# Kernel optimization log

Hardware: AMD Instinct MI355X
Metric: run time of the kernel (lower is better)

Reference implementation:

```python
import jax, jax.numpy as jnp
import numpy as np
from jax import lax

NEG = -1e9
B, H, C, TX, TY = 4, 256, 80, 256, 1024  # batch, hidden, mel bins, text len, mel len


def setup_inputs() -> dict:
    key = jax.random.key(0)
    k = jax.random.split(key, 6)
    en = jax.random.normal(k[0], (B, H, TX), jnp.float32)
    mu = jax.random.normal(k[1], (B, C, TX), jnp.float32)
    log_sigma = 0.1 * jax.random.normal(k[2], (B, C, TX), jnp.float32)
    y = jax.random.normal(k[3], (B, C, TY), jnp.float32)
    x_lengths = jax.random.randint(k[4], (B,), TX // 2, TX + 1, jnp.int32)
    y_lengths = jax.random.randint(k[5], (B,), TY // 2, TY + 1, jnp.int32)
    return {"en": en, "mu": mu, "log_sigma": log_sigma, "y": y,
            "x_lengths": x_lengths, "y_lengths": y_lengths}


def sequence_mask(lengths, max_len):
    return jnp.arange(max_len)[None, :] < lengths[:, None]


def compute_log_probs(mu, log_sigma, y):
    # y: [B,C,Ty] -> [B,1,Ty,C]; mu/log_sigma: [B,C,Tx] -> [B,Tx,1,C]
    yb = jnp.transpose(y, (0, 2, 1))[:, None]
    mub = jnp.transpose(mu, (0, 2, 1))[:, :, None]
    lsb = jnp.transpose(log_sigma, (0, 2, 1))[:, :, None]
    # mse / sigma^2 = (y-mu)^2 * exp(-2*log_sigma); mean over channel dim
    expo = -0.5 * jnp.mean((yb - mub) ** 2 * jnp.exp(-2.0 * lsb), axis=-1)  # [B,Tx,Ty]
    return expo - 0.5 * jnp.mean(lsb, axis=-1)  # broadcast [B,Tx,1] -> [B,Tx,Ty]


def maximum_path(logp, mask, x_lengths, y_lengths):
    """Monotonic alignment search (Glow-TTS Viterbi DP), vectorized over batch."""
    b, tx, ty = logp.shape
    lp = jnp.where(mask > 0, logp, NEG)
    cols = jnp.moveaxis(lp, 2, 0)  # [Ty, B, Tx]
    v0 = jnp.broadcast_to(jnp.where(jnp.arange(tx) == 0, 0.0, NEG), (b, tx)).astype(logp.dtype)

    def fwd(v, col):
        v_shift = jnp.concatenate([jnp.full((b, 1), NEG, v.dtype), v[:, :-1]], axis=1)
        diag = v_shift > v  # come from (x-1, y-1) rather than (x, y-1)
        return col + jnp.maximum(v, v_shift), diag

    _, diags = lax.scan(fwd, v0, cols)  # diags: [Ty, B, Tx] bool

    xs_idx = jnp.arange(tx)

    def bwd(idx, inp):
        yv, dcol = inp
        active = yv < y_lengths  # [B]
        row = (xs_idx[None, :] == idx[:, None]) & active[:, None]
        d = jnp.take_along_axis(dcol, idx[:, None], axis=1)[:, 0]
        idx = jnp.where(active & (idx > 0) & d, idx - 1, idx)
        return idx, row

    _, rows = lax.scan(bwd, x_lengths - 1, (jnp.arange(ty), diags), reverse=True)
    return lax.stop_gradient(jnp.moveaxis(rows, 0, 2).astype(logp.dtype))  # [B,Tx,Ty]


def generate_path(dr, mask):
    # dr: [B,Tx] durations; mask: [B,Tx,Ty]
    ty = mask.shape[-1]
    cum = jnp.cumsum(dr, axis=1)
    pm = (jnp.arange(ty)[None, None, :] < cum[:, :, None]).astype(dr.dtype)
    path = pm - jnp.pad(pm, ((0, 0), (1, 0), (0, 0)))[:, :-1]
    return path * mask


def reference(en, mu, log_sigma, y, x_lengths, y_lengths):
    tx, ty = mu.shape[-1], y.shape[-1]
    x_mask = sequence_mask(x_lengths, tx).astype(jnp.float32)  # [B,Tx]
    y_mask = sequence_mask(y_lengths, ty).astype(jnp.float32)  # [B,Ty]
    attn_mask = x_mask[:, :, None] * y_mask[:, None, :]        # [B,Tx,Ty]
    logp = compute_log_probs(mu, log_sigma, y)
    attn = maximum_path(logp, attn_mask, x_lengths, y_lengths)
    dr_mas = jnp.sum(attn, axis=-1)                            # durations [B,Tx]
    path = generate_path(dr_mas, attn_mask)                    # convert_dr_to_align
    # expand_encoder_outputs: attn^T @ en^T -> [B,H,Ty]
    o_en_ex = jnp.einsum('bxy,bhx->bhy', path, en)
    return o_en_ex, logp, attn, dr_mas
```

## Files before the change

### kernel.cpp

```cpp
#include <hip/hip_runtime.h>
#include <cstdint>
#include <cmath>

#define B_ 4
#define H_ 256
#define C_ 80
#define TX_ 256
#define TY_ 1024
#define NC_ 64
#define NEGF (-1e9f)

#define OFF_LOGP (B_*H_*TY_)
#define OFF_ATTN (OFF_LOGP + B_*TX_*TY_)
#define OFF_DR   (OFF_ATTN + B_*TX_*TY_)

__device__ __forceinline__ float dpp_shr1_negfill_f32(float x) {
  union { float f; int i; } u, o, r;
  u.f = x; o.f = NEGF;
  r.i = __builtin_amdgcn_update_dpp(o.i, u.i, 0x138, 0xf, 0xf, false);
  return r.f;
}

__global__ __launch_bounds__(256) void k_logp(
    const float* __restrict__ mu, const float* __restrict__ ls,
    const float* __restrict__ y, const int* __restrict__ xlp,
    const int* __restrict__ ylp, float* __restrict__ logp_out,
    float* __restrict__ lpT)
{
  const int b  = blockIdx.y;
  const int x0 = blockIdx.x * 4;
  const int tid = threadIdx.x;
  __shared__ double s_w[4][C_];
  __shared__ double s_m1[4][C_];
  __shared__ double s_wm2[4][C_];
  __shared__ double s_lsv[4][C_];
  __shared__ double s_K[4];
  __shared__ double s_t0[4];
  __shared__ float tile[TY_][4];
  for (int i = tid; i < 4 * C_; i += 256) {
    int xi = i / C_, c = i - xi * C_;
    double m = (double)mu[(b * C_ + c) * TX_ + x0 + xi];
    double l = (double)ls[(b * C_ + c) * TX_ + x0 + xi];
    double w = exp(-2.0 * l);
    s_w[xi][c]   = w;
    s_m1[xi][c]  = -2.0 * w * m;
    s_wm2[xi][c] = w * m * m;
    s_lsv[xi][c] = l;
  }
  __syncthreads();
  {
    int xi = tid >> 6, cc = tid & 63;
    double kp = (cc < C_) ? s_wm2[xi][cc] : 0.0;
    double tp = (cc < C_) ? s_lsv[xi][cc] : 0.0;
    if (cc + 64 < C_) { kp += s_wm2[xi][cc + 64]; tp += s_lsv[xi][cc + 64]; }
#pragma unroll
    for (int off = 32; off; off >>= 1) {
      kp += __shfl_down(kp, off);
      tp += __shfl_down(tp, off);
    }
    if (cc == 0) { s_K[xi] = kp; s_t0[xi] = -0.5 * (tp * (1.0 / C_)); }
  }
  __syncthreads();

  const int t0 = tid * 4;
  double acc[4][4];
#pragma unroll
  for (int xi = 0; xi < 4; ++xi)
#pragma unroll
    for (int k = 0; k < 4; ++k) acc[xi][k] = 0.0;

  const float4* yp = (const float4*)(y + (size_t)b * C_ * TY_) + tid;
#pragma unroll 4
  for (int c = 0; c < C_; ++c) {
    float4 yv = yp[c * (TY_ / 4)];
    double y0 = yv.x, y1 = yv.y, y2 = yv.z, y3 = yv.w;
#pragma unroll
    for (int xi = 0; xi < 4; ++xi) {
      double w = s_w[xi][c], m1 = s_m1[xi][c];
      double u0 = fma(w, y0, m1), u1 = fma(w, y1, m1);
      double u2 = fma(w, y2, m1), u3 = fma(w, y3, m1);
      acc[xi][0] = fma(u0, y0, acc[xi][0]);
      acc[xi][1] = fma(u1, y1, acc[xi][1]);
      acc[xi][2] = fma(u2, y2, acc[xi][2]);
      acc[xi][3] = fma(u3, y3, acc[xi][3]);
    }
  }

  const int xlen = xlp[b], ylen = ylp[b];
#pragma unroll
  for (int xi = 0; xi < 4; ++xi) {
    int x = x0 + xi;
    double c0 = s_t0[xi], K = s_K[xi];
    float r[4];
#pragma unroll
    for (int k = 0; k < 4; ++k)
      r[k] = (float)((acc[xi][k] + K) * (-0.5 / C_) + c0);
    *(float4*)&logp_out[((size_t)(b * TX_ + x)) * TY_ + t0] =
        make_float4(r[0], r[1], r[2], r[3]);
    bool xm = x < xlen;
#pragma unroll
    for (int k = 0; k < 4; ++k)
      tile[t0 + k][xi] = (xm && (t0 + k) < ylen) ? r[k] : NEGF;
  }
  __syncthreads();

  float* dst = lpT + (size_t)b * TY_ * TX_ + x0;
  const float4* tp = (const float4*)tile;
#pragma unroll
  for (int k = 0; k < 4; ++k) {
    int t = tid + 256 * k;
    *(float4*)&dst[(size_t)t * TX_] = tp[t];
  }
}

#define PHASE_BAR() \
  asm volatile("s_waitcnt lgkmcnt(0)\n\ts_barrier" ::: "memory")

#define PHASEQ(FL, FC, q)                                                   \
  {                                                                         \
    const int cl = (q) - w;                                                 \
    if (cl >= 0 && cl < NC_) {                                              \
      const float* cb = gb + (size_t)cl * 16 * TX_ + tid;                   \
      _Pragma("unroll")                                                     \
      for (int i = 0; i < 16; ++i) FL[i] = cb[i * TX_];                     \
    }                                                                       \
    const int cc = (q) - 2 - w;                                             \
    if (cc >= 0 && cc < NC_) {                                              \
      if (cc == 0) { v = (tid == 0) ? 0.0f : NEGF; word = 0u; }             \
      const uint32_t bitbase = 1u << ((cc & 1) << 4);                       \
      float* wr = (lane == 63) ? &bdry[cc & 1][w + 1][0] : &dummy[lane];    \
      const float* bp = &bdry[cc & 1][w][0];                                \
      float bv[16];                                                         \
      *(float4*)&bv[0]  = *(const float4*)(bp);                             \
      *(float4*)&bv[4]  = *(const float4*)(bp + 4);                         \
      *(float4*)&bv[8]  = *(const float4*)(bp + 8);                         \
      *(float4*)&bv[12] = *(const float4*)(bp + 12);                        \
      wr[0] = v;                                                            \
      _Pragma("unroll")                                                     \
      for (int i = 0; i < 16; ++i) {                                        \
        float vl = dpp_shr1_negfill_f32(v);                                 \
        if (amlane0) vl = bv[i];                                            \
        if (vl > v) word |= (bitbase << i);                                 \
        float nv = FC[i] + fmaxf(v, vl);                                    \
        if (i < 15) wr[i + 1] = nv;                                         \
        v = nv;                                                             \
      }                                                                     \
      if (cc & 1) { bits[(cc >> 1) * 256 + tid] = word; word = 0u; }        \
    }                                                                       \
    PHASE_BAR();                                                            \
  }

__global__ __launch_bounds__(256, 1) void k_dp(
    const float* __restrict__ lpT, const int* __restrict__ xlp,
    const int* __restrict__ ylp, float* __restrict__ dr_out,
    int* __restrict__ cum_ws, int* __restrict__ xt_ws)
{
  const int b = blockIdx.x;
  const int tid = threadIdx.x;
  const int lane = tid & 63;
  const int w = tid >> 6;
  __shared__ uint32_t bits[8192];
  __shared__ uint32_t dur[TX_];
  __shared__ float bdry[2][5][16];
  __shared__ float dummy[80];

  const float* gb = lpT + (size_t)b * TY_ * TX_;
  const bool amlane0 = (w > 0) && (lane == 0);

  float v = NEGF;
  uint32_t word = 0;
  float f0[16], f1[16], f2[16];

  for (int q = 0; q < 69; q += 3) {
    PHASEQ(f0, f1, q);
    PHASEQ(f1, f2, q + 1);
    PHASEQ(f2, f0, q + 2);
  }
  __syncthreads();

  dur[tid] = 0;
  __syncthreads();

  const int xlen = xlp[b], ylen = ylp[b];
  if (tid == 0) {
    int idx = xlen - 1;
    int t = ylen - 1;
    while (t >= 0) {
      if (idx == 0) { dur[0] = (uint32_t)(t + 1); break; }
      int ww = t >> 5, rr = t & 31;
      uint32_t wd = bits[ww * 256 + idx];
      wd &= (rr == 31) ? 0xffffffffu : ((1u << (rr + 1)) - 1u);
      while (wd == 0 && ww > 0) { --ww; wd = bits[ww * 256 + idx]; }
      if (wd == 0) { dur[idx] = (uint32_t)(t + 1); break; }
      int bitpos = 31 - __builtin_clz(wd);
      int tp = (ww << 5) | bitpos;
      dur[idx] = (uint32_t)(t - tp + 1);
      --idx;
      t = tp - 1;
    }
  }
  __syncthreads();

  if (w == 0) {
    uint32_t d0 = dur[4 * lane], d1 = dur[4 * lane + 1];
    uint32_t d2 = dur[4 * lane + 2], d3 = dur[4 * lane + 3];
    uint32_t own = d0 + d1 + d2 + d3;
    uint32_t s = own;
#pragma unroll
    for (int off = 1; off < 64; off <<= 1) {
      uint32_t n = __shfl_up(s, off);
      if (lane >= off) s += n;
    }
    uint32_t base = s - own;
    uint32_t c0 = base + d0, c1 = c0 + d1, c2 = c1 + d2, c3 = c2 + d3;
    int x = 4 * lane;
    cum_ws[b * TX_ + x]     = (int)c0;
    cum_ws[b * TX_ + x + 1] = (int)c1;
    cum_ws[b * TX_ + x + 2] = (int)c2;
    cum_ws[b * TX_ + x + 3] = (int)c3;
    dr_out[b * TX_ + x]     = (float)d0;
    dr_out[b * TX_ + x + 1] = (float)d1;
    dr_out[b * TX_ + x + 2] = (float)d2;
    dr_out[b * TX_ + x + 3] = (float)d3;
    int* xt = xt_ws + b * TY_;
    for (uint32_t t = c0 - d0; t < c0; ++t) xt[t] = x;
    for (uint32_t t = c1 - d1; t < c1; ++t) xt[t] = x + 1;
    for (uint32_t t = c2 - d2; t < c2; ++t) xt[t] = x + 2;
    for (uint32_t t = c3 - d3; t < c3; ++t) xt[t] = x + 3;
  }
}

__global__ __launch_bounds__(256) void k_epi(
    const int* __restrict__ cum_ws, const int* __restrict__ xt_ws,
    const float* __restrict__ en, const int* __restrict__ ylp,
    float* __restrict__ attn, float* __restrict__ oen)
{
  const int b = blockIdx.y, bx = blockIdx.x, tid = threadIdx.x;
  __shared__ float row[TX_];
  if (bx < TX_) {
    const int x = bx;
    int hi = cum_ws[b * TX_ + x];
    int lo = (x > 0) ? cum_ws[b * TX_ + x - 1] : 0;
    int t0 = tid * 4;
    float4 v;
    v.x = (t0     >= lo && t0     < hi) ? 1.f : 0.f;
    v.y = (t0 + 1 >= lo && t0 + 1 < hi) ? 1.f : 0.f;
    v.z = (t0 + 2 >= lo && t0 + 2 < hi) ? 1.f : 0.f;
    v.w = (t0 + 3 >= lo && t0 + 3 < hi) ? 1.f : 0.f;
    *(float4*)&attn[((size_t)(b * TX_ + x)) * TY_ + t0] = v;
  } else {
    const int h = bx - TX_;
    row[tid] = en[((size_t)(b * H_ + h)) * TX_ + tid];
    __syncthreads();
    const int ylen = ylp[b];
    int t0 = tid * 4;
    int4 xi = *(const int4*)&xt_ws[b * TY_ + t0];
    float4 v;
    v.x = (t0     < ylen) ? row[xi.x & (TX_ - 1)] : 0.f;
    v.y = (t0 + 1 < ylen) ? row[xi.y & (TX_ - 1)] : 0.f;
    v.z = (t0 + 2 < ylen) ? row[xi.z & (TX_ - 1)] : 0.f;
    v.w = (t0 + 3 < ylen) ? row[xi.w & (TX_ - 1)] : 0.f;
    *(float4*)&oen[((size_t)(b * H_ + h)) * TY_ + t0] = v;
  }
}

extern "C" void kernel_launch(void* const* d_in, const int* in_sizes, int n_in,
                              void* d_out, int out_size, void* d_ws, size_t ws_size,
                              hipStream_t stream)
{
  const float* en = (const float*)d_in[0];
  const float* mu = (const float*)d_in[1];
  const float* ls = (const float*)d_in[2];
  const float* y  = (const float*)d_in[3];
  const int*   xl = (const int*)d_in[4];
  const int*   yl = (const int*)d_in[5];

  float* out  = (float*)d_out;
  float* oen  = out;
  float* logp = out + OFF_LOGP;
  float* attn = out + OFF_ATTN;
  float* dr   = out + OFF_DR;

  int* cum = (int*)d_ws;
  int* xt  = cum + B_ * TX_;

  k_logp<<<dim3(TX_ / 4, B_),   256, 0, stream>>>(mu, ls, y, xl, yl, logp, attn);
  k_dp  <<<B_,                  256, 0, stream>>>(attn, xl, yl, dr, cum, xt);
  k_epi <<<dim3(TX_ + H_, B_),  256, 0, stream>>>(cum, xt, en, yl, attn, oen);
}
```

Before: 188.1 us.

## Double DP wavefront chunk size to halve barrier phases

Each wave in the wavefront DP now processes 32 mel columns per phase instead of 16, cutting the phase count from 69 to 39 and so the number of block-wide barriers. Boundary values are buffered in registers and written by lane 63 as float4 stores rather than per-step scalar writes to a dummy array, and each phase stores its own full 32-bit backpointer word. Loads are clamped instead of branched. The backtrack also prefetches the previous bitmask word speculatively. In exchange the pipeline fill and drain stages get longer and register pressure roughly doubles (three 32-float buffers), which risks spills.

Result: slower. 200.0 us (+6.3%).

```diff
diff --git a/kernel.cpp b/kernel.cpp
--- a/kernel.cpp
+++ b/kernel.cpp
@@ -7,7 +7,7 @@
 #define C_ 80
 #define TX_ 256
 #define TY_ 1024
-#define NC_ 64
+#define NCH_ 32
 #define NEGF (-1e9f)
 
 #define OFF_LOGP (B_*H_*TY_)
@@ -119,33 +119,37 @@
 #define PHASEQ(FL, FC, q)                                                   \
   {                                                                         \
     const int cl = (q) - w;                                                 \
-    if (cl >= 0 && cl < NC_) {                                              \
-      const float* cb = gb + (size_t)cl * 16 * TX_ + tid;                   \
+    const int clc = cl < 0 ? 0 : (cl >= NCH_ ? NCH_ - 1 : cl);              \
+    const float* cb = gb + (size_t)clc * 32 * TX_ + tid;                    \
+    _Pragma("unroll")                                                       \
+    for (int i = 0; i < 32; ++i) FL[i] = cb[i * TX_];    \
+    const int cc = (q) - 2 - w;                                             \
+    if (cc >= 0 && cc < NCH_) {                                             \
+      if (cc == 0) v = (tid == 0) ? 0.0f : NEGF;                            \
+      uint32_t word = 0u;                                                   \
+      const float* bp = &bdry[cc & 1][w][0];                                \
+      float bv[32];                                                         \
       _Pragma("unroll")                                                     \
-      for (int i = 0; i < 16; ++i) FL[i] = cb[i * TX_];                     \
-    }                                                                       \
-    const int cc = (q) - 2 - w;                                             \
-    if (cc >= 0 && cc < NC_) {                                              \
-      if (cc == 0) { v = (tid == 0) ? 0.0f : NEGF; word = 0u; }             \
-      const uint32_t bitbase = 1u << ((cc & 1) << 4);                       \
-      float* wr = (lane == 63) ? &bdry[cc & 1][w + 1][0] : &dummy[lane];    \
-      const float* bp = &bdry[cc & 1][w][0];                                \
-      float bv[16];                                                         \
-      *(float4*)&bv[0]  = *(const float4*)(bp);                             \
-      *(float4*)&bv[4]  = *(const float4*)(bp + 4);                         \
-      *(float4*)&bv[8]  = *(const float4*)(bp + 8);                         \
-      *(float4*)&bv[12] = *(const float4*)(bp + 12);                        \
-      wr[0] = v;                                                            \
+      for (int i = 0; i < 8; ++i)                                           \
+        *(float4*)&bv[4 * i] = *(const float4*)(bp + 4 * i);                \
+      float bs[32];                                                         \
+      bs[0] = v;                                                            \
       _Pragma("unroll")                                                     \
-      for (int i = 0; i < 16; ++i) {                                        \
+      for (int i = 0; i < 32; ++i) {                                        \
         float vl = dpp_shr1_negfill_f32(v);                                 \
         if (amlane0) vl = bv[i];                                            \
-        if (vl > v) word |= (bitbase << i);                                 \
+        if (vl > v) word |= (1u << i);                                      \
         float nv = FC[i] + fmaxf(v, vl);                                    \
-        if (i < 15) wr[i + 1] = nv;                                         \
+        if (i < 31) bs[i + 1] = nv;                                         \
         v = nv;                                                             \
       }                                                                     \
-      if (cc & 1) { bits[(cc >> 1) * 256 + tid] = word; word = 0u; }        \
+      if (lane == 63) {                                                     \
+        float* wr = &bdry[cc & 1][w + 1][0];                                \
+        _Pragma("unroll")                                                   \
+        for (int i = 0; i < 8; ++i)                                         \
+          *(float4*)(wr + 4 * i) = *(float4*)&bs[4 * i];                    \
+      }                                                                     \
+      bits[cc * 256 + tid] = word;                                          \
     }                                                                       \
     PHASE_BAR();                                                            \
   }
@@ -161,17 +165,15 @@
   const int w = tid >> 6;
   __shared__ uint32_t bits[8192];
   __shared__ uint32_t dur[TX_];
-  __shared__ float bdry[2][5][16];
-  __shared__ float dummy[80];
+  __shared__ float bdry[2][5][32];
 
   const float* gb = lpT + (size_t)b * TY_ * TX_;
   const bool amlane0 = (w > 0) && (lane == 0);
 
   float v = NEGF;
-  uint32_t word = 0;
-  float f0[16], f1[16], f2[16];
-
-  for (int q = 0; q < 69; q += 3) {
+  float f0[32], f1[32], f2[32];
+
+  for (int q = 0; q < 39; q += 3) {
     PHASEQ(f0, f1, q);
     PHASEQ(f1, f2, q + 1);
     PHASEQ(f2, f0, q + 2);
@@ -188,12 +190,16 @@
     while (t >= 0) {
       if (idx == 0) { dur[0] = (uint32_t)(t + 1); break; }
       int ww = t >> 5, rr = t & 31;
-      uint32_t wd = bits[ww * 256 + idx];
-      wd &= (rr == 31) ? 0xffffffffu : ((1u << (rr + 1)) - 1u);
-      while (wd == 0 && ww > 0) { --ww; wd = bits[ww * 256 + idx]; }
+      uint32_t w0 = bits[ww * 256 + idx];
+      uint32_t w1 = (ww > 0) ? bits[(ww - 1) * 256 + idx] : 0u;
+      w0 &= (rr == 31) ? 0xffffffffu : ((1u << (rr + 1)) - 1u);
+      uint32_t wd = w0;
+      int wsel = ww;
+      if (wd == 0) { wd = w1; wsel = ww - 1; }
+      while (wd == 0 && wsel > 0) { --wsel; wd = bits[wsel * 256 + idx]; }
       if (wd == 0) { dur[idx] = (uint32_t)(t + 1); break; }
       int bitpos = 31 - __builtin_clz(wd);
-      int tp = (ww << 5) | bitpos;
+      int tp = (wsel << 5) | bitpos;
       dur[idx] = (uint32_t)(t - tp + 1);
       --idx;
       t = tp - 1;
```
